# Performance work log

Hardware: AMD Instinct MI355X
Metric: run time of the kernel (lower is better)

The kernel has to match this reference:

```python
import jax, jax.numpy as jnp
import numpy as np

JITTER_EPS = 0.01  # router_jitter_noise from PhiMoEConfig


def phi_routing(logits, jitter_eps=JITTER_EPS):
    # masked-sampling top-2 routing used by PhiMoESparseMoeBlock (inference path)
    m, sel = jax.lax.top_k(logits, 2)          # [T,2] values / indices
    T, E = logits.shape
    # --- first expert gate ---
    m1 = m[:, :1]
    factor1 = jnp.maximum(jnp.abs(logits), m1)
    mask1 = (m1 - logits) / factor1 > 2.0 * jitter_eps
    p1 = jax.nn.softmax(jnp.where(mask1, -jnp.inf, logits), axis=-1)
    mult1 = jnp.take_along_axis(p1, sel[:, :1], axis=-1)
    # --- second expert gate (first selected expert removed) ---
    m2 = m[:, 1:2]
    factor2 = jnp.maximum(jnp.abs(logits), m2)
    mask2 = (m2 - logits) / factor2 > 2.0 * jitter_eps
    drop_top1 = jnp.arange(E)[None, :] == sel[:, :1]
    p2 = jax.nn.softmax(jnp.where(mask2 | drop_top1, -jnp.inf, logits), axis=-1)
    mult2 = jnp.take_along_axis(p2, sel[:, 1:2], axis=-1)
    return jnp.concatenate([mult1, mult2], axis=-1), sel  # [T,2], [T,2]


def setup_inputs() -> dict:
    key = jax.random.key(0)
    k = jax.random.split(key, 5)
    B, S, H, F, E = 1, 512, 1024, 4096, 8
    return {
        "hidden_states": jax.random.normal(k[0], (B, S, H), jnp.float32),
        "gate_w": jax.random.normal(k[1], (E, H), jnp.float32) * 0.02,
        "w1": jax.random.normal(k[2], (E, F, H), jnp.float32) * 0.02,  # nn.Linear(H->F) weight [F,H]
        "w2": jax.random.normal(k[3], (E, H, F), jnp.float32) * 0.02,  # nn.Linear(F->H) weight [H,F]
        "w3": jax.random.normal(k[4], (E, F, H), jnp.float32) * 0.02,
    }


def reference(hidden_states, gate_w, w1, w2, w3):
    B, S, H = hidden_states.shape
    E = w1.shape[0]
    x = hidden_states.reshape(-1, H)                      # [T,H]
    logits = x @ gate_w.T                                 # [T,E] router logits
    routing_weights, selected = phi_routing(logits)       # [T,2]
    T = x.shape[0]
    # dense per-token expert weight matrix [T,E]; zero weight == token not routed
    wte = jnp.zeros((T, E), x.dtype).at[jnp.arange(T)[:, None], selected].add(routing_weights)
    out = jnp.zeros_like(x)
    for e in range(E):  # small fixed expert count; SwiGLU expert MLP
        h = jax.nn.silu(x @ w1[e].T) * (x @ w3[e].T)      # [T,F]
        out = out + wte[:, e:e + 1] * (h @ w2[e].T)       # weighted combine
    return out.reshape(B, S, H)
```

## Files before the change

kernel.cpp:

```cpp
#include <hip/hip_runtime.h>
#include <hip/hip_bf16.h>

#define T_TOK 512
#define H_DIM 1024
#define F_DIM 4096
#define NEXP  8

typedef __attribute__((ext_vector_type(8))) short bf16x8;
typedef __attribute__((ext_vector_type(4))) float f32x4;

__device__ __forceinline__ short f2bs(float f) {
    __hip_bfloat16 h = __float2bfloat16(f);
    return __builtin_bit_cast(short, h);
}

__global__ __launch_bounds__(256) void routing_kernel(
    const float* __restrict__ x, const float* __restrict__ gw,
    int* __restrict__ cnt, int* __restrict__ tok, float* __restrict__ wgt,
    __hip_bfloat16* __restrict__ xbf)
{
    int wave = threadIdx.x >> 6, lane = threadIdx.x & 63;
    int t = blockIdx.x * 4 + wave;
    const float* xr = x + (size_t)t * H_DIM;

    float xv[16];
    #pragma unroll
    for (int j = 0; j < 16; ++j) xv[j] = xr[lane + 64 * j];
    #pragma unroll
    for (int j = 0; j < 16; ++j)
        xbf[(size_t)t * H_DIM + lane + 64 * j] = __float2bfloat16(xv[j]);

    float lg[8];
    #pragma unroll
    for (int e = 0; e < 8; ++e) {
        const float* g = gw + (size_t)e * H_DIM;
        float s = 0.f;
        #pragma unroll
        for (int j = 0; j < 16; ++j) s += xv[j] * g[lane + 64 * j];
        #pragma unroll
        for (int d = 1; d < 64; d <<= 1) s += __shfl_xor(s, d);
        lg[e] = s;
    }

    float m1 = -1e30f; int i1 = 0;
    #pragma unroll
    for (int e = 0; e < 8; ++e) if (lg[e] > m1) { m1 = lg[e]; i1 = e; }
    float m2 = -1e30f; int i2 = 0;
    #pragma unroll
    for (int e = 0; e < 8; ++e) if (e != i1 && lg[e] > m2) { m2 = lg[e]; i2 = e; }

    float s1 = 0.f, s2 = 0.f;
    #pragma unroll
    for (int e = 0; e < 8; ++e) {
        float fac1 = fmaxf(fabsf(lg[e]), m1);
        if (!((m1 - lg[e]) / fac1 > 0.02f)) s1 += expf(lg[e] - m1);
        if (e != i1) {
            float fac2 = fmaxf(fabsf(lg[e]), m2);
            if (!((m2 - lg[e]) / fac2 > 0.02f)) s2 += expf(lg[e] - m2);
        }
    }
    if (lane == 0) {
        float mult1 = 1.f / s1, mult2 = 1.f / s2;
        int p1 = atomicAdd(&cnt[i1], 1);
        tok[i1 * T_TOK + p1] = t; wgt[i1 * T_TOK + p1] = mult1;
        int p2 = atomicAdd(&cnt[i2], 1);
        tok[i2 * T_TOK + p2] = t; wgt[i2 * T_TOK + p2] = mult2;
    }
}

__global__ __launch_bounds__(256) void ffn1_kernel(
    const float* __restrict__ w1, const float* __restrict__ w3,
    const __hip_bfloat16* __restrict__ xbf,
    __hip_bfloat16* __restrict__ hbuf,
    const int* __restrict__ cnt, const int* __restrict__ tok)
{
    int e = blockIdx.y;
    int c[8];
    #pragma unroll
    for (int j = 0; j < 8; ++j) c[j] = cnt[j];
    int nt = c[e];
    int offE = 0;
    #pragma unroll
    for (int j = 0; j < 8; ++j) if (j < e) offE += c[j];

    int m0 = blockIdx.z * 256;
    if (m0 >= nt) return;
    int nact = min(nt - m0, 256);
    int f0 = blockIdx.x * 32;

    int wv = threadIdx.x >> 6, lane = threadIdx.x & 63;
    int lr = lane & 15, kg = lane >> 4;

    int rem = nact - wv * 64;
    int actn = (rem <= 0) ? 0 : min((rem + 15) >> 4, 4);
    if (actn == 0) return;

    const __hip_bfloat16* ap[4];
    #pragma unroll
    for (int mi = 0; mi < 4; ++mi) {
        int row = m0 + wv * 64 + mi * 16 + lr;
        int rc = min(row, nt - 1);
        int tt = tok[e * T_TOK + rc];
        ap[mi] = xbf + (size_t)tt * H_DIM + kg * 8;
    }
    const float* bp[4];
    const float* w1e = w1 + (size_t)e * F_DIM * H_DIM;
    const float* w3e = w3 + (size_t)e * F_DIM * H_DIM;
    #pragma unroll
    for (int ni = 0; ni < 2; ++ni) {
        bp[ni]     = w1e + (size_t)(f0 + ni * 16 + lr) * H_DIM + kg * 8;
        bp[ni + 2] = w3e + (size_t)(f0 + ni * 16 + lr) * H_DIM + kg * 8;
    }

    f32x4 acc[4][4];
    #pragma unroll
    for (int mi = 0; mi < 4; ++mi)
        #pragma unroll
        for (int ni = 0; ni < 4; ++ni) acc[mi][ni] = (f32x4){0.f, 0.f, 0.f, 0.f};

    auto load_ab = [&](bf16x8* a, bf16x8* b, int kk) {
        #pragma unroll
        for (int mi = 0; mi < 4; ++mi)
            a[mi] = *reinterpret_cast<const bf16x8*>(ap[mi] + kk);
        #pragma unroll
        for (int ni = 0; ni < 4; ++ni) {
            f32x4 lo = *reinterpret_cast<const f32x4*>(bp[ni] + kk);
            f32x4 hi = *reinterpret_cast<const f32x4*>(bp[ni] + kk + 4);
            bf16x8 tb;
            #pragma unroll
            for (int j = 0; j < 4; ++j) { tb[j] = f2bs(lo[j]); tb[4 + j] = f2bs(hi[j]); }
            b[ni] = tb;
        }
    };
    auto do_mfma = [&](bf16x8* a, bf16x8* b) {
        #pragma unroll
        for (int mi = 0; mi < 4; ++mi) {
            if (mi >= actn) break;
            #pragma unroll
            for (int ni = 0; ni < 4; ++ni)
                acc[mi][ni] = __builtin_amdgcn_mfma_f32_16x16x32_bf16(a[mi], b[ni], acc[mi][ni], 0, 0, 0);
        }
    };

    bf16x8 a0[4], b0[4], a1[4], b1[4];
    load_ab(a0, b0, 0);
    for (int k = 0; k < H_DIM; k += 64) {
        load_ab(a1, b1, k + 32);
        do_mfma(a0, b0);
        if (k + 64 < H_DIM) load_ab(a0, b0, k + 64);
        do_mfma(a1, b1);
    }

    #pragma unroll
    for (int mi = 0; mi < 4; ++mi) {
        if (mi >= actn) break;
        #pragma unroll
        for (int ni = 0; ni < 2; ++ni) {
            f32x4 d1 = acc[mi][ni], d3 = acc[mi][ni + 2];
            int fc = f0 + ni * 16 + lr;
            #pragma unroll
            for (int r = 0; r < 4; ++r) {
                int rl = wv * 64 + mi * 16 + kg * 4 + r;
                if (rl < nact) {
                    float v1 = d1[r];
                    float hv = (v1 / (1.f + expf(-v1))) * d3[r];
                    hbuf[(size_t)(offE + m0 + rl) * F_DIM + fc] = __float2bfloat16(hv);
                }
            }
        }
    }
}

__global__ __launch_bounds__(256) void ffn2_kernel(
    const float* __restrict__ w2,
    const __hip_bfloat16* __restrict__ hbuf,
    const int* __restrict__ cnt, const int* __restrict__ tok,
    const float* __restrict__ wgt,
    float* __restrict__ out)
{
    int e = blockIdx.y;
    int c[8];
    #pragma unroll
    for (int j = 0; j < 8; ++j) c[j] = cnt[j];
    int nt = c[e];
    int offE = 0;
    #pragma unroll
    for (int j = 0; j < 8; ++j) if (j < e) offE += c[j];

    int mt = blockIdx.z >> 1, ks = blockIdx.z & 1;
    int m0 = mt * 256;
    if (m0 >= nt) return;
    int nact = min(nt - m0, 256);
    int n0 = blockIdx.x * 64;

    int wv = threadIdx.x >> 6, lane = threadIdx.x & 63;
    int lr = lane & 15, kg = lane >> 4;

    int rem = nact - wv * 64;
    int actn = (rem <= 0) ? 0 : min((rem + 15) >> 4, 4);
    if (actn == 0) return;

    const __hip_bfloat16* ap[4];
    #pragma unroll
    for (int mi = 0; mi < 4; ++mi) {
        int rl = wv * 64 + mi * 16 + lr;
        int rc = min(rl, nact - 1);
        ap[mi] = hbuf + (size_t)(offE + m0 + rc) * F_DIM + kg * 8;
    }
    const float* bp[4];
    const float* w2e = w2 + (size_t)e * H_DIM * F_DIM;
    #pragma unroll
    for (int ni = 0; ni < 4; ++ni)
        bp[ni] = w2e + (size_t)(n0 + ni * 16 + lr) * F_DIM + kg * 8;

    f32x4 acc[4][4];
    #pragma unroll
    for (int mi = 0; mi < 4; ++mi)
        #pragma unroll
        for (int ni = 0; ni < 4; ++ni) acc[mi][ni] = (f32x4){0.f, 0.f, 0.f, 0.f};

    auto load_ab = [&](bf16x8* a, bf16x8* b, int kk) {
        #pragma unroll
        for (int mi = 0; mi < 4; ++mi)
            a[mi] = *reinterpret_cast<const bf16x8*>(ap[mi] + kk);
        #pragma unroll
        for (int ni = 0; ni < 4; ++ni) {
            f32x4 lo = *reinterpret_cast<const f32x4*>(bp[ni] + kk);
            f32x4 hi = *reinterpret_cast<const f32x4*>(bp[ni] + kk + 4);
            bf16x8 tb;
            #pragma unroll
            for (int j = 0; j < 4; ++j) { tb[j] = f2bs(lo[j]); tb[4 + j] = f2bs(hi[j]); }
            b[ni] = tb;
        }
    };
    auto do_mfma = [&](bf16x8* a, bf16x8* b) {
        #pragma unroll
        for (int mi = 0; mi < 4; ++mi) {
            if (mi >= actn) break;
            #pragma unroll
            for (int ni = 0; ni < 4; ++ni)
                acc[mi][ni] = __builtin_amdgcn_mfma_f32_16x16x32_bf16(a[mi], b[ni], acc[mi][ni], 0, 0, 0);
        }
    };

    int kbeg = ks * 2048, kend = kbeg + 2048;
    bf16x8 a0[4], b0[4], a1[4], b1[4];
    load_ab(a0, b0, kbeg);
    for (int k = kbeg; k < kend; k += 64) {
        load_ab(a1, b1, k + 32);
        do_mfma(a0, b0);
        if (k + 64 < kend) load_ab(a0, b0, k + 64);
        do_mfma(a1, b1);
    }

    #pragma unroll
    for (int mi = 0; mi < 4; ++mi) {
        if (mi >= actn) break;
        #pragma unroll
        for (int ni = 0; ni < 4; ++ni) {
            f32x4 d = acc[mi][ni];
            int col = n0 + ni * 16 + lr;
            #pragma unroll
            for (int r = 0; r < 4; ++r) {
                int rl = wv * 64 + mi * 16 + kg * 4 + r;
                if (rl < nact) {
                    int sl = m0 + rl;
                    int tt = tok[e * T_TOK + sl];
                    float wvv = wgt[e * T_TOK + sl];
                    atomicAdd(&out[(size_t)tt * H_DIM + col], wvv * d[r]);
                }
            }
        }
    }
}

extern "C" void kernel_launch(void* const* d_in, const int* in_sizes, int n_in,
                              void* d_out, int out_size, void* d_ws, size_t ws_size,
                              hipStream_t stream)
{
    const float* x  = (const float*)d_in[0];
    const float* gw = (const float*)d_in[1];
    const float* w1 = (const float*)d_in[2];
    const float* w2 = (const float*)d_in[3];
    const float* w3 = (const float*)d_in[4];
    float* out = (float*)d_out;

    char* ws = (char*)d_ws;
    int*   cnt = (int*)(ws);
    int*   tok = (int*)(ws + 256);
    float* wgt = (float*)(ws + 16640);
    __hip_bfloat16* xbf  = (__hip_bfloat16*)(ws + 33280);
    __hip_bfloat16* hbuf = (__hip_bfloat16*)(ws + 1081856);

    hipMemsetAsync(cnt, 0, 256, stream);
    hipMemsetAsync(out, 0, (size_t)out_size * sizeof(float), stream);

    routing_kernel<<<dim3(T_TOK / 4), 256, 0, stream>>>(x, gw, cnt, tok, wgt, xbf);
    ffn1_kernel<<<dim3(F_DIM / 32, NEXP, 2), 256, 0, stream>>>(w1, w3, xbf, hbuf, cnt, tok);
    ffn2_kernel<<<dim3(H_DIM / 64, NEXP, 4), 256, 0, stream>>>(w2, hbuf, cnt, tok, wgt, out);
}
```

Measured before the change: 494.9 us.

## Stage fp32 expert weights into swizzled LDS via async global-to-LDS double buffering

Both FFN kernels now copy the fp32 weight tiles into a double-buffered, XOR-swizzled shared-memory buffer using global_load_lds. Each wave then reads its B fragments from LDS instead of issuing its own per-lane global loads, so the weight tile is fetched once per block and shared by all four waves. ffn2's K dimension is split four ways instead of two to create more blocks, and both kernels gain a launch_bounds occupancy hint. The cost is added __syncthreads per k-step, 32KB of LDS per block, and more atomic traffic into the output from the extra K split.

```diff
diff --git a/kernel.cpp b/kernel.cpp
--- a/kernel.cpp
+++ b/kernel.cpp
@@ -13,6 +13,11 @@
     __hip_bfloat16 h = __float2bfloat16(f);
     return __builtin_bit_cast(short, h);
 }
+
+#define GLOAD_LDS16(SRC, DST)                                                              \
+    __builtin_amdgcn_global_load_lds(                                                      \
+        (const __attribute__((address_space(1))) unsigned int*)(SRC),                      \
+        (__attribute__((address_space(3))) unsigned int*)(DST), 16, 0, 0)
 
 __global__ __launch_bounds__(256) void routing_kernel(
     const float* __restrict__ x, const float* __restrict__ gw,
@@ -68,12 +73,14 @@
     }
 }
 
-__global__ __launch_bounds__(256) void ffn1_kernel(
+__global__ __launch_bounds__(256, 3) void ffn1_kernel(
     const float* __restrict__ w1, const float* __restrict__ w3,
     const __hip_bfloat16* __restrict__ xbf,
     __hip_bfloat16* __restrict__ hbuf,
     const int* __restrict__ cnt, const int* __restrict__ tok)
 {
+    __shared__ char sm[32768];
+
     int e = blockIdx.y;
     int c[8];
     #pragma unroll
@@ -88,12 +95,14 @@
     int nact = min(nt - m0, 256);
     int f0 = blockIdx.x * 32;
 
-    int wv = threadIdx.x >> 6, lane = threadIdx.x & 63;
+    int tid = threadIdx.x;
+    int wv = tid >> 6, lane = tid & 63;
     int lr = lane & 15, kg = lane >> 4;
-
     int rem = nact - wv * 64;
     int actn = (rem <= 0) ? 0 : min((rem + 15) >> 4, 4);
-    if (actn == 0) return;
+
+    const float* w1e = w1 + (size_t)e * F_DIM * H_DIM;
+    const float* w3e = w3 + (size_t)e * F_DIM * H_DIM;
 
     const __hip_bfloat16* ap[4];
     #pragma unroll
@@ -103,14 +112,24 @@
         int tt = tok[e * T_TOK + rc];
         ap[mi] = xbf + (size_t)tt * H_DIM + kg * 8;
     }
-    const float* bp[4];
-    const float* w1e = w1 + (size_t)e * F_DIM * H_DIM;
-    const float* w3e = w3 + (size_t)e * F_DIM * H_DIM;
-    #pragma unroll
-    for (int ni = 0; ni < 2; ++ni) {
-        bp[ni]     = w1e + (size_t)(f0 + ni * 16 + lr) * H_DIM + kg * 8;
-        bp[ni + 2] = w3e + (size_t)(f0 + ni * 16 + lr) * H_DIM + kg * 8;
-    }
+
+    const float* sb[4];
+    int dstL[4];
+    #pragma unroll
+    for (int i = 0; i < 4; ++i) {
+        int r = i * 16 + (tid >> 4);
+        int cb = ((tid & 15) << 4) ^ ((r & 7) << 5);
+        const float* base = (r < 32) ? w1e + (size_t)(f0 + r) * H_DIM
+                                     : w3e + (size_t)(f0 + r - 32) * H_DIM;
+        sb[i] = base + (cb >> 2);
+        dstL[i] = i * 4096 + tid * 16;
+    }
+
+    auto STAGE = [&](int buf, int kt) {
+        #pragma unroll
+        for (int i = 0; i < 4; ++i)
+            GLOAD_LDS16(sb[i] + kt * 64, sm + buf * 16384 + dstL[i]);
+    };
 
     f32x4 acc[4][4];
     #pragma unroll
@@ -118,37 +137,42 @@
         #pragma unroll
         for (int ni = 0; ni < 4; ++ni) acc[mi][ni] = (f32x4){0.f, 0.f, 0.f, 0.f};
 
-    auto load_ab = [&](bf16x8* a, bf16x8* b, int kk) {
-        #pragma unroll
-        for (int mi = 0; mi < 4; ++mi)
-            a[mi] = *reinterpret_cast<const bf16x8*>(ap[mi] + kk);
-        #pragma unroll
-        for (int ni = 0; ni < 4; ++ni) {
-            f32x4 lo = *reinterpret_cast<const f32x4*>(bp[ni] + kk);
-            f32x4 hi = *reinterpret_cast<const f32x4*>(bp[ni] + kk + 4);
-            bf16x8 tb;
-            #pragma unroll
-            for (int j = 0; j < 4; ++j) { tb[j] = f2bs(lo[j]); tb[4 + j] = f2bs(hi[j]); }
-            b[ni] = tb;
-        }
-    };
-    auto do_mfma = [&](bf16x8* a, bf16x8* b) {
-        #pragma unroll
-        for (int mi = 0; mi < 4; ++mi) {
-            if (mi >= actn) break;
-            #pragma unroll
-            for (int ni = 0; ni < 4; ++ni)
-                acc[mi][ni] = __builtin_amdgcn_mfma_f32_16x16x32_bf16(a[mi], b[ni], acc[mi][ni], 0, 0, 0);
-        }
-    };
-
-    bf16x8 a0[4], b0[4], a1[4], b1[4];
-    load_ab(a0, b0, 0);
-    for (int k = 0; k < H_DIM; k += 64) {
-        load_ab(a1, b1, k + 32);
-        do_mfma(a0, b0);
-        if (k + 64 < H_DIM) load_ab(a0, b0, k + 64);
-        do_mfma(a1, b1);
+    STAGE(0, 0);
+    __syncthreads();
+    int cur = 0;
+
+    for (int kt = 0; kt < 16; ++kt) {
+        bf16x8 av[2][4];
+        if (actn) {
+            #pragma unroll
+            for (int ks = 0; ks < 2; ++ks)
+                #pragma unroll
+                for (int mi = 0; mi < 4; ++mi)
+                    av[ks][mi] = *reinterpret_cast<const bf16x8*>(ap[mi] + kt * 64 + ks * 32);
+        }
+        if (kt < 15) STAGE(cur ^ 1, kt + 1);
+        if (actn) {
+            const char* bb = sm + cur * 16384;
+            #pragma unroll
+            for (int ks = 0; ks < 2; ++ks) {
+                #pragma unroll
+                for (int ni = 0; ni < 4; ++ni) {
+                    int r = ni * 16 + lr;
+                    const char* p = bb + r * 256 + (((ks * 128 + kg * 32)) ^ ((r & 7) << 5));
+                    f32x4 lo = *reinterpret_cast<const f32x4*>(p);
+                    f32x4 hi = *reinterpret_cast<const f32x4*>(p + 16);
+                    bf16x8 bv;
+                    #pragma unroll
+                    for (int j = 0; j < 4; ++j) { bv[j] = f2bs(lo[j]); bv[4 + j] = f2bs(hi[j]); }
+                    #pragma unroll
+                    for (int mi = 0; mi < 4; ++mi)
+                        if (mi < actn)
+                            acc[mi][ni] = __builtin_amdgcn_mfma_f32_16x16x32_bf16(av[ks][mi], bv, acc[mi][ni], 0, 0, 0);
+                }
+            }
+        }
+        __syncthreads();
+        cur ^= 1;
     }
 
     #pragma unroll
@@ -171,13 +195,15 @@
     }
 }
 
-__global__ __launch_bounds__(256) void ffn2_kernel(
+__global__ __launch_bounds__(256, 3) void ffn2_kernel(
     const float* __restrict__ w2,
     const __hip_bfloat16* __restrict__ hbuf,
     const int* __restrict__ cnt, const int* __restrict__ tok,
     const float* __restrict__ wgt,
     float* __restrict__ out)
 {
+    __shared__ char sm[32768];
+
     int e = blockIdx.y;
     int c[8];
     #pragma unroll
@@ -187,31 +213,45 @@
     #pragma unroll
     for (int j = 0; j < 8; ++j) if (j < e) offE += c[j];
 
-    int mt = blockIdx.z >> 1, ks = blockIdx.z & 1;
+    int z = blockIdx.z;
+    int ks4 = z & 3, mt = z >> 2;
     int m0 = mt * 256;
     if (m0 >= nt) return;
     int nact = min(nt - m0, 256);
     int n0 = blockIdx.x * 64;
-
-    int wv = threadIdx.x >> 6, lane = threadIdx.x & 63;
+    int kbeg = ks4 * 1024;
+
+    int tid = threadIdx.x;
+    int wv = tid >> 6, lane = tid & 63;
     int lr = lane & 15, kg = lane >> 4;
-
     int rem = nact - wv * 64;
     int actn = (rem <= 0) ? 0 : min((rem + 15) >> 4, 4);
-    if (actn == 0) return;
+
+    const float* w2e = w2 + (size_t)e * H_DIM * F_DIM;
 
     const __hip_bfloat16* ap[4];
     #pragma unroll
     for (int mi = 0; mi < 4; ++mi) {
         int rl = wv * 64 + mi * 16 + lr;
         int rc = min(rl, nact - 1);
-        ap[mi] = hbuf + (size_t)(offE + m0 + rc) * F_DIM + kg * 8;
-    }
-    const float* bp[4];
-    const float* w2e = w2 + (size_t)e * H_DIM * F_DIM;
-    #pragma unroll
-    for (int ni = 0; ni < 4; ++ni)
-        bp[ni] = w2e + (size_t)(n0 + ni * 16 + lr) * F_DIM + kg * 8;
+        ap[mi] = hbuf + (size_t)(offE + m0 + rc) * F_DIM + kbeg + kg * 8;
+    }
+
+    const float* sb[4];
+    int dstL[4];
+    #pragma unroll
+    for (int i = 0; i < 4; ++i) {
+        int r = i * 16 + (tid >> 4);
+        int cb = ((tid & 15) << 4) ^ ((r & 7) << 5);
+        sb[i] = w2e + (size_t)(n0 + r) * F_DIM + kbeg + (cb >> 2);
+        dstL[i] = i * 4096 + tid * 16;
+    }
+
+    auto STAGE = [&](int buf, int kt) {
+        #pragma unroll
+        for (int i = 0; i < 4; ++i)
+            GLOAD_LDS16(sb[i] + kt * 64, sm + buf * 16384 + dstL[i]);
+    };
 
     f32x4 acc[4][4];
     #pragma unroll
@@ -219,38 +259,42 @@
         #pragma unroll
         for (int ni = 0; ni < 4; ++ni) acc[mi][ni] = (f32x4){0.f, 0.f, 0.f, 0.f};
 
-    auto load_ab = [&](bf16x8* a, bf16x8* b, int kk) {
-        #pragma unroll
-        for (int mi = 0; mi < 4; ++mi)
-            a[mi] = *reinterpret_cast<const bf16x8*>(ap[mi] + kk);
-        #pragma unroll
-        for (int ni = 0; ni < 4; ++ni) {
-            f32x4 lo = *reinterpret_cast<const f32x4*>(bp[ni] + kk);
-            f32x4 hi = *reinterpret_cast<const f32x4*>(bp[ni] + kk + 4);
-            bf16x8 tb;
-            #pragma unroll
-            for (int j = 0; j < 4; ++j) { tb[j] = f2bs(lo[j]); tb[4 + j] = f2bs(hi[j]); }
-            b[ni] = tb;
-        }
-    };
-    auto do_mfma = [&](bf16x8* a, bf16x8* b) {
-        #pragma unroll
-        for (int mi = 0; mi < 4; ++mi) {
-            if (mi >= actn) break;
-            #pragma unroll
-            for (int ni = 0; ni < 4; ++ni)
-                acc[mi][ni] = __builtin_amdgcn_mfma_f32_16x16x32_bf16(a[mi], b[ni], acc[mi][ni], 0, 0, 0);
-        }
-    };
-
-    int kbeg = ks * 2048, kend = kbeg + 2048;
-    bf16x8 a0[4], b0[4], a1[4], b1[4];
-    load_ab(a0, b0, kbeg);
-    for (int k = kbeg; k < kend; k += 64) {
-        load_ab(a1, b1, k + 32);
-        do_mfma(a0, b0);
-        if (k + 64 < kend) load_ab(a0, b0, k + 64);
-        do_mfma(a1, b1);
+    STAGE(0, 0);
+    __syncthreads();
+    int cur = 0;
+
+    for (int kt = 0; kt < 16; ++kt) {
+        bf16x8 av[2][4];
+        if (actn) {
+            #pragma unroll
+            for (int ks = 0; ks < 2; ++ks)
+                #pragma unroll
+                for (int mi = 0; mi < 4; ++mi)
+                    av[ks][mi] = *reinterpret_cast<const bf16x8*>(ap[mi] + kt * 64 + ks * 32);
+        }
+        if (kt < 15) STAGE(cur ^ 1, kt + 1);
+        if (actn) {
+            const char* bb = sm + cur * 16384;
+            #pragma unroll
+            for (int ks = 0; ks < 2; ++ks) {
+                #pragma unroll
+                for (int ni = 0; ni < 4; ++ni) {
+                    int r = ni * 16 + lr;
+                    const char* p = bb + r * 256 + (((ks * 128 + kg * 32)) ^ ((r & 7) << 5));
+                    f32x4 lo = *reinterpret_cast<const f32x4*>(p);
+                    f32x4 hi = *reinterpret_cast<const f32x4*>(p + 16);
+                    bf16x8 bv;
+                    #pragma unroll
+                    for (int j = 0; j < 4; ++j) { bv[j] = f2bs(lo[j]); bv[4 + j] = f2bs(hi[j]); }
+                    #pragma unroll
+                    for (int mi = 0; mi < 4; ++mi)
+                        if (mi < actn)
+                            acc[mi][ni] = __builtin_amdgcn_mfma_f32_16x16x32_bf16(av[ks][mi], bv, acc[mi][ni], 0, 0, 0);
+                }
+            }
+        }
+        __syncthreads();
+        cur ^= 1;
     }
 
     #pragma unroll
@@ -297,5 +341,5 @@
 
     routing_kernel<<<dim3(T_TOK / 4), 256, 0, stream>>>(x, gw, cnt, tok, wgt, xbf);
     ffn1_kernel<<<dim3(F_DIM / 32, NEXP, 2), 256, 0, stream>>>(w1, w3, xbf, hbuf, cnt, tok);
-    ffn2_kernel<<<dim3(H_DIM / 64, NEXP, 4), 256, 0, stream>>>(w2, hbuf, cnt, tok, wgt, out);
-}
+    ffn2_kernel<<<dim3(H_DIM / 64, NEXP, 8), 256, 0, stream>>>(w2, hbuf, cnt, tok, wgt, out);
+}
```

Result: faster. 449.6 us (-9.2%).
